# Optimization experiments

Hardware: AMD Instinct MI355X
Metric: run time of the kernel (lower is better)

Reference implementation:

```python
import jax, jax.numpy as jnp
import numpy as np

EPS = 1e-9


def setup_inputs() -> dict:
    key = jax.random.key(0)
    ks = jax.random.split(key, 6)
    B, L, D = 4096, 100, 64
    return {
        "candidate": jax.random.normal(ks[0], (B, 1, D), dtype=jnp.float32),
        "clicks": jax.random.normal(ks[1], (B, L, D), dtype=jnp.float32),
        "mask": jax.random.randint(ks[2], (B, L), 0, 2, dtype=jnp.int32),
        "W1": jax.random.normal(ks[3], (4 * D, 64), dtype=jnp.float32) * 0.05,
        "b1": jnp.zeros((64,), dtype=jnp.float32),
        "alpha": jnp.zeros((64,), dtype=jnp.float32),
        "W2": jax.random.normal(ks[4], (64, 1), dtype=jnp.float32) * 0.05,
        "b2": jnp.zeros((1,), dtype=jnp.float32),
    }


def reference(candidate, clicks, mask, W1, b1, alpha, W2, b2):
    B, L, D = clicks.shape
    cand = jnp.broadcast_to(candidate, (B, L, D))
    # attention_input: [B, L, 4D]
    x = jnp.concatenate([cand, clicks, cand - clicks, cand * clicks], axis=-1)
    x = x.reshape(B * L, 4 * D)
    # Linear(4D -> 64)
    h = x @ W1 + b1  # [B*L, 64]
    # Dice: BatchNorm1d (affine=False, training-mode batch stats) + learned alpha
    mu = jnp.mean(h, axis=0)
    var = jnp.mean(jnp.square(h - mu), axis=0)  # biased var, as in BN normalization
    hn = (h - mu) * jax.lax.rsqrt(var + EPS)
    p = jax.nn.sigmoid(hn)
    d = p * h + (1.0 - p) * alpha * h
    # Linear(64 -> 1)
    w = (d @ W2 + b2).reshape(B, L)
    m = mask.astype(w.dtype)
    w = w * m
    w = w + (-1e9) * (1.0 - m)  # din_use_softmax=True masking
    w = jax.nn.softmax(w, axis=-1)
    # weighted sum over clicks: [B, D]
    out = jnp.einsum("bl,bld->bd", w, clicks)
    return out
```

## Files before the change

### kernel.cpp

```cpp
#include <hip/hip_runtime.h>


constexpr int Bn = 4096;
constexpr int Ln = 100;
constexpr int LP = 112;
constexpr float kEps = 1e-9f;
constexpr int NBUCK = 16;

typedef _Float16 half8 __attribute__((ext_vector_type(8)));
typedef __attribute__((ext_vector_type(4))) float f32x4;

static __device__ __forceinline__ int swz(int row, int byteInRow) {
  return row * 128 + (byteInRow ^ ((row & 7) << 4));
}

template <int PHASE>
__global__ __launch_bounds__(256) void din_kernel(
    const float* __restrict__ cand, const float* __restrict__ clicks,
    const int* __restrict__ mask, const float* __restrict__ W1,
    const float* __restrict__ b1, const float* __restrict__ alpha,
    const float* __restrict__ W2, const float* __restrict__ b2,
    float* __restrict__ ws, float* __restrict__ out) {
  __shared__ alignas(16) _Float16 AS[LP * 64];
  __shared__ alignas(16) _Float16 MS[64 * 64];
  __shared__ float cshS[64];
  __shared__ float cuS[64];
  __shared__ float scratchS[4][LP];
  __shared__ float s_lds[LP];
  __shared__ float w_lds[LP];

  const int b = blockIdx.x;
  const int tid = threadIdx.x;
  const int lane = tid & 63;
  const int w = tid >> 6;

  if (tid < 64) cshS[tid] = cand[(size_t)b * 64 + tid];
  __syncthreads();

  {
    float cuacc = 0.f;
#pragma unroll
    for (int p = 0; p < 8; ++p) {
      const int i0 = w * 16 + p * 2;
      float m[2];
#pragma unroll
      for (int q = 0; q < 2; ++q) {
        const int i = i0 + q;
        const float ci = cshS[i];
        m[q] = W1[(64 + i) * 64 + lane] - W1[(128 + i) * 64 + lane] +
               ci * W1[(192 + i) * 64 + lane];
        cuacc = fmaf(ci, W1[i * 64 + lane] + W1[(128 + i) * 64 + lane], cuacc);
      }
      auto pk = __builtin_amdgcn_cvt_pkrtz(m[0], m[1]);
      *(decltype(pk)*)((char*)MS + swz(lane, i0 * 2)) = pk;
    }
    scratchS[w][lane] = cuacc;
  }

  {
    const float2* crow2 = (const float2*)(clicks + (size_t)b * Ln * 64);
    const int colh = lane & 31;
    const int rsel = lane >> 5;
#pragma unroll
    for (int it = 0; it < 14; ++it) {
      const int l = 28 * w + it * 2 + rsel;
      float v0 = 0.f, v1 = 0.f;
      if (l < Ln) {
        float2 v = crow2[l * 32 + colh];
        v0 = v.x;
        v1 = v.y;
      }
      auto pk = __builtin_amdgcn_cvt_pkrtz(v0, v1);
      *(decltype(pk)*)((char*)AS + swz(l, colh * 4)) = pk;
    }
  }
  __syncthreads();
  if (tid < 64)
    cuS[tid] = b1[tid] + scratchS[0][tid] + scratchS[1][tid] +
               scratchS[2][tid] + scratchS[3][tid];
  __syncthreads();

  const int lo4 = lane & 15;
  const int hi2 = lane >> 4;
  const int bk2 = hi2 * 16;
  const int bcol = w * 16 + lo4;

  half8 B0 = *(const half8*)((char*)MS + swz(bcol, bk2));
  half8 B1 = *(const half8*)((char*)MS + swz(bcol, 64 + bk2));

  f32x4 acc[7];
#pragma unroll
  for (int rt = 0; rt < 7; ++rt) acc[rt] = (f32x4){0.f, 0.f, 0.f, 0.f};

#pragma unroll
  for (int rt = 0; rt < 7; ++rt) {
    const int arow = rt * 16 + lo4;
    half8 A0 = *(const half8*)((char*)AS + swz(arow, bk2));
    half8 A1 = *(const half8*)((char*)AS + swz(arow, 64 + bk2));
    f32x4 a = acc[rt];
    a = __builtin_amdgcn_mfma_f32_16x16x32_f16(A0, B0, a, 0, 0, 0);
    a = __builtin_amdgcn_mfma_f32_16x16x32_f16(A1, B1, a, 0, 0, 0);
    acc[rt] = a;
  }

  const int j = w * 16 + lo4;
  const float cuj = cuS[j];

  if (PHASE == 0) {
    float ssum = 0.f, ssq = 0.f;
#pragma unroll
    for (int rt = 0; rt < 7; ++rt) {
#pragma unroll
      for (int r = 0; r < 4; ++r) {
        const int l = rt * 16 + hi2 * 4 + r;
        const float h = acc[rt][r] + cuj;
        if (l < Ln) {
          ssum += h;
          ssq = fmaf(h, h, ssq);
        }
      }
    }
    ssum += __shfl_xor(ssum, 16);
    ssum += __shfl_xor(ssum, 32);
    ssq += __shfl_xor(ssq, 16);
    ssq += __shfl_xor(ssq, 32);
    if (hi2 == 0) {
      atomicAdd(&ws[(b & (NBUCK - 1)) * 128 + j], ssum);
      atomicAdd(&ws[(b & (NBUCK - 1)) * 128 + 64 + j], ssq);
    }
  } else {
    const float muj = ws[2048 + j];
    const float rsj = ws[2112 + j];
    const float aj = alpha[j];
    const float w2j = W2[j];
    const float b2v = b2[0];
#pragma unroll
    for (int rt = 0; rt < 7; ++rt) {
#pragma unroll
      for (int r = 0; r < 4; ++r) {
        const int l = rt * 16 + hi2 * 4 + r;
        const float h = acc[rt][r] + cuj;
        const float hn = (h - muj) * rsj;
        const float p = 1.f / (1.f + __expf(-hn));
        const float d = h * fmaf(p, 1.f - aj, aj);
        float sv = d * w2j;
        sv += __shfl_xor(sv, 1);
        sv += __shfl_xor(sv, 2);
        sv += __shfl_xor(sv, 4);
        sv += __shfl_xor(sv, 8);
        if (lo4 == 0) scratchS[w][l] = sv;
      }
    }
    __syncthreads();
    if (tid < LP)
      s_lds[tid] = b2v + scratchS[0][tid] + scratchS[1][tid] +
                   scratchS[2][tid] + scratchS[3][tid];
    __syncthreads();

    if (w == 0) {
      const int* mrow = mask + (size_t)b * Ln;
      const bool has1 = (lane + 64) < Ln;
      float v0 = s_lds[lane];
      int m0 = mrow[lane];
      float v1 = has1 ? s_lds[lane + 64] : 0.f;
      int m1 = has1 ? mrow[lane + 64] : 0;
      float x0 = m0 ? v0 : -3.0e38f;
      float x1 = m1 ? v1 : -3.0e38f;
      float mx = fmaxf(x0, x1);
#pragma unroll
      for (int off = 32; off >= 1; off >>= 1) mx = fmaxf(mx, __shfl_xor(mx, off));
      float e0 = m0 ? __expf(v0 - mx) : 0.f;
      float e1 = m1 ? __expf(v1 - mx) : 0.f;
      float se = e0 + e1;
#pragma unroll
      for (int off = 32; off >= 1; off >>= 1) se += __shfl_xor(se, off);
      float inv = 1.f / se;
      w_lds[lane] = e0 * inv;
      if (has1) w_lds[lane + 64] = e1 * inv;
    }
    __syncthreads();

    float acco = 0.f;
#pragma unroll
    for (int t = 0; t < 25; ++t) {
      const int l = w + 4 * t;
      const float wl = w_lds[l];
      const _Float16 kv = *(const _Float16*)((char*)AS + swz(l, lane * 2));
      acco = fmaf(wl, (float)kv, acco);
    }
    scratchS[w][lane] = acco;
    __syncthreads();
    if (w == 0)
      out[(size_t)b * 64 + lane] = scratchS[0][lane] + scratchS[1][lane] +
                                   scratchS[2][lane] + scratchS[3][lane];
  }
}

__global__ void finalize_stats(float* __restrict__ ws) {
  int j = threadIdx.x;
  float s = 0.f, q = 0.f;
#pragma unroll
  for (int k = 0; k < NBUCK; ++k) {
    s += ws[k * 128 + j];
    q += ws[k * 128 + 64 + j];
  }
  const float n = (float)(Bn * Ln);
  float mu = s / n;
  float var = q / n - mu * mu;
  ws[2048 + j] = mu;
  ws[2112 + j] = rsqrtf(var + kEps);
}

extern "C" void kernel_launch(void* const* d_in, const int* in_sizes, int n_in,
                              void* d_out, int out_size, void* d_ws,
                              size_t ws_size, hipStream_t stream) {
  const float* cand = (const float*)d_in[0];
  const float* clicks = (const float*)d_in[1];
  const int* mask = (const int*)d_in[2];
  const float* W1 = (const float*)d_in[3];
  const float* b1 = (const float*)d_in[4];
  const float* alpha = (const float*)d_in[5];
  const float* W2 = (const float*)d_in[6];
  const float* b2 = (const float*)d_in[7];
  float* out = (float*)d_out;
  float* ws = (float*)d_ws;

  (void)hipMemsetAsync(d_ws, 0, NBUCK * 128 * sizeof(float), stream);
  din_kernel<0><<<Bn, 256, 0, stream>>>(cand, clicks, mask, W1, b1, alpha, W2,
                                        b2, ws, out);
  finalize_stats<<<1, 64, 0, stream>>>(ws);
  din_kernel<1><<<Bn, 256, 0, stream>>>(cand, clicks, mask, W1, b1, alpha, W2,
                                        b2, ws, out);
}
```

Before: 261.8 us.

## Cache pre-activation h in fp16 workspace and use lightweight second pass

The first pass now writes the hidden pre-activations h as fp16 into workspace, and a new lite kernel computes Dice, softmax and the weighted sum from h without recomputing W1 preprocessing or the MFMA GEMM. The clicks load is also changed to float4 vector loads. This trades extra global traffic (writing and re-reading h) for removing recomputation in the second pass. It falls back to the old path if the workspace is too small.

```diff
diff --git a/kernel.cpp b/kernel.cpp
--- a/kernel.cpp
+++ b/kernel.cpp
@@ -6,6 +6,7 @@
 constexpr int LP = 112;
 constexpr float kEps = 1e-9f;
 constexpr int NBUCK = 16;
+constexpr size_t H_OFF_FLOATS = 2176;
 
 typedef _Float16 half8 __attribute__((ext_vector_type(8)));
 typedef __attribute__((ext_vector_type(4))) float f32x4;
@@ -14,13 +15,14 @@
   return row * 128 + (byteInRow ^ ((row & 7) << 4));
 }
 
-template <int PHASE>
+template <int PHASE, bool STOREH>
 __global__ __launch_bounds__(256) void din_kernel(
     const float* __restrict__ cand, const float* __restrict__ clicks,
     const int* __restrict__ mask, const float* __restrict__ W1,
     const float* __restrict__ b1, const float* __restrict__ alpha,
     const float* __restrict__ W2, const float* __restrict__ b2,
-    float* __restrict__ ws, float* __restrict__ out) {
+    float* __restrict__ ws, _Float16* __restrict__ hbuf,
+    float* __restrict__ out) {
   __shared__ alignas(16) _Float16 AS[LP * 64];
   __shared__ alignas(16) _Float16 MS[64 * 64];
   __shared__ float cshS[64];
@@ -58,20 +60,23 @@
   }
 
   {
-    const float2* crow2 = (const float2*)(clicks + (size_t)b * Ln * 64);
-    const int colh = lane & 31;
-    const int rsel = lane >> 5;
-#pragma unroll
-    for (int it = 0; it < 14; ++it) {
-      const int l = 28 * w + it * 2 + rsel;
-      float v0 = 0.f, v1 = 0.f;
-      if (l < Ln) {
-        float2 v = crow2[l * 32 + colh];
-        v0 = v.x;
-        v1 = v.y;
-      }
-      auto pk = __builtin_amdgcn_cvt_pkrtz(v0, v1);
-      *(decltype(pk)*)((char*)AS + swz(l, colh * 4)) = pk;
+    const float4* crow4 = (const float4*)(clicks + (size_t)b * Ln * 64);
+    const int r16 = tid >> 4;
+    const int c4 = tid & 15;
+#pragma unroll
+    for (int it = 0; it < 7; ++it) {
+      const int l = it * 16 + r16;
+      float4 v = {0.f, 0.f, 0.f, 0.f};
+      if (l < Ln) v = crow4[l * 16 + c4];
+      auto p0 = __builtin_amdgcn_cvt_pkrtz(v.x, v.y);
+      auto p1 = __builtin_amdgcn_cvt_pkrtz(v.z, v.w);
+      unsigned u0, u1;
+      __builtin_memcpy(&u0, &p0, 4);
+      __builtin_memcpy(&u1, &p1, 4);
+      uint2 uv;
+      uv.x = u0;
+      uv.y = u1;
+      *(uint2*)((char*)AS + swz(l, c4 * 8)) = uv;
     }
   }
   __syncthreads();
@@ -107,6 +112,7 @@
   const float cuj = cuS[j];
 
   if (PHASE == 0) {
+    _Float16* hb = hbuf + (size_t)b * Ln * 64 + j;
     float ssum = 0.f, ssq = 0.f;
 #pragma unroll
     for (int rt = 0; rt < 7; ++rt) {
@@ -117,6 +123,7 @@
         if (l < Ln) {
           ssum += h;
           ssq = fmaf(h, h, ssq);
+          if (STOREH) hb[(size_t)l * 64] = (_Float16)h;
         }
       }
     }
@@ -196,6 +203,79 @@
   }
 }
 
+__global__ __launch_bounds__(256) void din_lite(
+    const float* __restrict__ clicks, const int* __restrict__ mask,
+    const float* __restrict__ alpha, const float* __restrict__ W2,
+    const float* __restrict__ b2, const float* __restrict__ ws,
+    const _Float16* __restrict__ hbuf, float* __restrict__ out) {
+  __shared__ float s_lds[LP];
+  __shared__ float w_lds[Ln];
+  __shared__ float scratchS[4][64];
+
+  const int b = blockIdx.x;
+  const int tid = threadIdx.x;
+  const int lane = tid & 63;
+  const int w = tid >> 6;
+
+  const float muj = ws[2048 + lane];
+  const float rsj = ws[2112 + lane];
+  const float aj = alpha[lane];
+  const float w2j = W2[lane];
+  const float b2v = b2[0];
+
+  const _Float16* hrow = hbuf + (size_t)b * Ln * 64 + lane;
+
+#pragma unroll 5
+  for (int t = 0; t < 25; ++t) {
+    const int l = w + 4 * t;
+    const float h = (float)hrow[(size_t)l * 64];
+    const float hn = (h - muj) * rsj;
+    const float p = 1.f / (1.f + __expf(-hn));
+    const float d = h * fmaf(p, 1.f - aj, aj);
+    float sv = d * w2j;
+#pragma unroll
+    for (int off = 32; off >= 1; off >>= 1) sv += __shfl_xor(sv, off);
+    if (lane == 0) s_lds[l] = sv + b2v;
+  }
+  __syncthreads();
+
+  if (w == 0) {
+    const int* mrow = mask + (size_t)b * Ln;
+    const bool has1 = (lane + 64) < Ln;
+    float v0 = s_lds[lane];
+    int m0 = mrow[lane];
+    float v1 = has1 ? s_lds[lane + 64] : 0.f;
+    int m1 = has1 ? mrow[lane + 64] : 0;
+    float x0 = m0 ? v0 : -3.0e38f;
+    float x1 = m1 ? v1 : -3.0e38f;
+    float mx = fmaxf(x0, x1);
+#pragma unroll
+    for (int off = 32; off >= 1; off >>= 1) mx = fmaxf(mx, __shfl_xor(mx, off));
+    float e0 = m0 ? __expf(v0 - mx) : 0.f;
+    float e1 = m1 ? __expf(v1 - mx) : 0.f;
+    float se = e0 + e1;
+#pragma unroll
+    for (int off = 32; off >= 1; off >>= 1) se += __shfl_xor(se, off);
+    float inv = 1.f / se;
+    w_lds[lane] = e0 * inv;
+    if (has1) w_lds[lane + 64] = e1 * inv;
+  }
+  __syncthreads();
+
+  const float* crow = clicks + (size_t)b * Ln * 64;
+  float acco = 0.f;
+#pragma unroll 5
+  for (int t = 0; t < 25; ++t) {
+    const int l = w + 4 * t;
+    acco = fmaf(w_lds[l], crow[(size_t)l * 64 + lane], acco);
+  }
+  scratchS[w][lane] = acco;
+  __syncthreads();
+  if (w == 0)
+    out[(size_t)b * 64 + lane] = scratchS[0][lane] + scratchS[1][lane] +
+                                 scratchS[2][lane] + scratchS[3][lane];
+}
+
 __global__ void finalize_stats(float* __restrict__ ws) {
   int j = threadIdx.x;
   float s = 0.f, q = 0.f;
@@ -224,11 +304,24 @@
   const float* b2 = (const float*)d_in[7];
   float* out = (float*)d_out;
   float* ws = (float*)d_ws;
+  _Float16* hbuf = (_Float16*)(ws + H_OFF_FLOATS);
+
+  const size_t need =
+      H_OFF_FLOATS * sizeof(float) + (size_t)Bn * Ln * 64 * sizeof(_Float16);
+  const bool fast = ws_size >= need;
 
   (void)hipMemsetAsync(d_ws, 0, NBUCK * 128 * sizeof(float), stream);
-  din_kernel<0><<<Bn, 256, 0, stream>>>(cand, clicks, mask, W1, b1, alpha, W2,
-                                        b2, ws, out);
-  finalize_stats<<<1, 64, 0, stream>>>(ws);
-  din_kernel<1><<<Bn, 256, 0, stream>>>(cand, clicks, mask, W1, b1, alpha, W2,
-                                        b2, ws, out);
-}
+  if (fast) {
+    din_kernel<0, true><<<Bn, 256, 0, stream>>>(cand, clicks, mask, W1, b1,
+                                                alpha, W2, b2, ws, hbuf, out);
+    finalize_stats<<<1, 64, 0, stream>>>(ws);
+    din_lite<<<Bn, 256, 0, stream>>>(clicks, mask, alpha, W2, b2, ws, hbuf,
+                                     out);
+  } else {
+    din_kernel<0, false><<<Bn, 256, 0, stream>>>(cand, clicks, mask, W1, b1,
+                                                 alpha, W2, b2, ws, hbuf, out);
+    finalize_stats<<<1, 64, 0, stream>>>(ws);
+    din_kernel<1, false><<<Bn, 256, 0, stream>>>(cand, clicks, mask, W1, b1,
+                                                 alpha, W2, b2, ws, hbuf, out);
+  }
+}
```

After: 236.1 us. -9.8%, faster.
